# Kernel optimization log

Measured on AMD Instinct MI355X. Metric: run time of the kernel, lower is better.

The kernel has to match this reference:

```python
import jax, jax.numpy as jnp
import numpy as np

B, C, LO, LQ, H = 64, 4, 64, 128, 768
NEG = -10000.0


def _trilinear(u, um, v, vm, w1, b1, w2, b2, w3):
    # u: [N, Lu, H], v: [N, Lv, H]; returns [N, Lu, Lv]
    p1 = u @ w1 + b1                                  # [N, Lu, 1]
    p2 = (v @ w2 + b2).transpose(0, 2, 1)             # [N, 1, Lv]
    p3 = jnp.einsum('bud,bvd->buv', u * w3, v)        # trilinear term
    return p1 + p2 + p3 + ((1.0 - um) * NEG)[:, :, None] + ((1.0 - vm) * NEG)[:, None, :]


def _forward(encoded_o, encoded_q, om, qm,
             att_W1_w, att_W1_b, att_W2_w, att_W2_b, att_W3,
             Wc_self_w, Wc_self_b, Wc_w, Wc_b, Va_w, Va_b, Wg_w, Wg_b,
             co_W1_w, co_W1_b, co_W2_w, co_W2_b, co_W3, Wp_w, Wp_b,
             sa_W1_w, sa_W1_b, sa_W2_w, sa_W2_b, sa_W3, Wf_w, Wf_b):
    b, c, lo, h = encoded_o.shape
    lq = encoded_q.shape[2]
    p = c * (c - 1)
    # ---- pairwise option-compare (OCN_Att_layer) over all (i, j), j != i ----
    i_idx = np.repeat(np.arange(c), c - 1)
    j_idx = np.array([j for i in range(c) for j in range(c) if j != i])
    o_i = encoded_o[:, i_idx].reshape(b * p, lo, h)   # 'ok'
    o_j = encoded_o[:, j_idx].reshape(b * p, lo, h)   # 'ol'
    m_i = om[:, i_idx].reshape(b * p, lo)
    m_j = om[:, j_idx].reshape(b * p, lo)
    A = _trilinear(o_j, m_j, o_i, m_i, att_W1_w, att_W1_b, att_W2_w, att_W2_b, att_W3)
    att = jax.nn.softmax(A, axis=1)
    olk_ctx = jnp.einsum('bud,buv->bvd', o_j, att)    # [BP, LO, H]
    OLK = jnp.concatenate([o_i - olk_ctx, o_i * olk_ctx], axis=-1)  # [BP, LO, 2H]
    cmp_proj = OLK @ Wc_w + Wc_b                      # Wc applied per compare pair
    cmp_sum = cmp_proj.reshape(b, c, c - 1, lo, h).sum(axis=2).reshape(b * c, lo, h)
    # ---- merge layer (per candidate, flattened into batch) ----
    o1 = encoded_o.reshape(b * c, lo, h)
    q = encoded_q.reshape(b * c, lq, h)
    omf = om.reshape(b * c, lo)
    qmf = qm.reshape(b * c, lq)
    Aq = jax.nn.softmax(q @ Va_w + Va_b + ((1.0 - qmf) * NEG)[:, :, None], axis=1)  # [BC, LQ, 1]
    Q = jnp.einsum('bld,blo->bod', q, Aq)             # [BC, 1, H]
    OCK = jnp.tanh(o1 @ Wc_self_w + Wc_self_b + cmp_sum)
    Qb = jnp.broadcast_to(Q, (b * c, lo, h))
    G = jax.nn.sigmoid(jnp.concatenate([o1, OCK, Qb], axis=-1) @ Wg_w + Wg_b)
    merged = G * o1 + (1.0 - G) * OCK                 # [BC, LO, H]
    # ---- co-attention with question ----
    A2 = _trilinear(q, qmf, merged, omf, co_W1_w, co_W1_b, co_W2_w, co_W2_b, co_W3)  # [BC, LQ, LO]
    ACK = jax.nn.softmax(A2, axis=2)
    OA = jnp.einsum('bqo,bod->bqd', ACK, merged)      # [BC, LQ, H]
    APK = jax.nn.softmax(A2, axis=1)
    dOA = jnp.concatenate([q, OA], axis=-1)           # [BC, LQ, 2H]
    POAA = jnp.einsum('bqd,bqo->bod', dOA, APK)       # [BC, LO, 2H]
    OPK = jax.nn.relu(jnp.concatenate([merged, POAA], axis=-1) @ Wp_w + Wp_b)
    # ---- self-attention ----
    A3 = _trilinear(OPK, omf, OPK, omf, sa_W1_w, sa_W1_b, sa_W2_w, sa_W2_b, sa_W3)
    att3 = jax.nn.softmax(A3, axis=1)
    OSK = jnp.einsum('bud,buv->bvd', OPK, att3)
    OFK = jax.nn.relu(jnp.concatenate([OPK, OSK, OPK - OSK, OPK * OSK], axis=-1) @ Wf_w + Wf_b)
    return OFK.reshape(b, c, lo, h).max(axis=2)       # [B, C, H]


def setup_inputs():
    ks = jax.random.split(jax.random.key(0), 32)
    def p(i, shape, s=0.02):
        return jax.random.normal(ks[i], shape, jnp.float32) * s
    return {
        'encoded_o': jax.random.normal(ks[0], (B, C, LO, H), jnp.float32),
        'encoded_q': jax.random.normal(ks[1], (B, C, LQ, H), jnp.float32),
        'option_mask': jnp.ones((B, C, LO), jnp.int32),
        'question_mask': jnp.ones((B, C, LQ), jnp.int32),
        'att_W1_w': p(2, (H, 1)), 'att_W1_b': p(3, (1,)),
        'att_W2_w': p(4, (H, 1)), 'att_W2_b': p(5, (1,)),
        'att_W3': p(6, (H,)),
        'Wc_self_w': p(7, (H, H)), 'Wc_self_b': p(8, (H,)),
        'Wc_w': p(9, (2 * H, H)), 'Wc_b': p(10, (H,)),
        'Va_w': p(11, (H, 1)), 'Va_b': p(12, (1,)),
        'Wg_w': p(13, (3 * H, H)), 'Wg_b': p(14, (H,)),
        'co_W1_w': p(15, (H, 1)), 'co_W1_b': p(16, (1,)),
        'co_W2_w': p(17, (H, 1)), 'co_W2_b': p(18, (1,)),
        'co_W3': p(19, (H,)),
        'Wp_w': p(20, (3 * H, H)), 'Wp_b': p(21, (H,)),
        'sa_W1_w': p(22, (H, 1)), 'sa_W1_b': p(23, (1,)),
        'sa_W2_w': p(24, (H, 1)), 'sa_W2_b': p(25, (1,)),
        'sa_W3': p(26, (H,)),
        'Wf_w': p(27, (4 * H, H)), 'Wf_b': p(28, (H,)),
    }


def reference(encoded_o, encoded_q, option_mask, question_mask,
              att_W1_w, att_W1_b, att_W2_w, att_W2_b, att_W3,
              Wc_self_w, Wc_self_b, Wc_w, Wc_b, Va_w, Va_b, Wg_w, Wg_b,
              co_W1_w, co_W1_b, co_W2_w, co_W2_b, co_W3, Wp_w, Wp_b,
              sa_W1_w, sa_W1_b, sa_W2_w, sa_W2_b, sa_W3, Wf_w, Wf_b):
    return _forward(encoded_o, encoded_q,
                    option_mask.astype(jnp.float32), question_mask.astype(jnp.float32),
                    att_W1_w, att_W1_b, att_W2_w, att_W2_b, att_W3,
                    Wc_self_w, Wc_self_b, Wc_w, Wc_b, Va_w, Va_b, Wg_w, Wg_b,
                    co_W1_w, co_W1_b, co_W2_w, co_W2_b, co_W3, Wp_w, Wp_b,
                    sa_W1_w, sa_W1_b, sa_W2_w, sa_W2_b, sa_W3, Wf_w, Wf_b)
```

## Files before the change

### kernel.cpp

```cpp
#include <hip/hip_runtime.h>
#include <math.h>


#define NEGC (-10000.0f)
constexpr int HD = 768;

constexpr int EP_TANH = 1;
constexpr int EP_MERGE = 2;
constexpr int EP_RELU = 3;
constexpr int EP_RELU_MAX = 4;

typedef __attribute__((ext_vector_type(8))) short bf16x8;
typedef __attribute__((ext_vector_type(8))) unsigned short u16x8;
typedef __attribute__((ext_vector_type(4))) unsigned short u16x4;
typedef __attribute__((ext_vector_type(4))) float f32x4;

__device__ inline void st8(float* dst, float4 a0, float4 a1) {
  dst[0] = a0.x; dst[1] = a0.y; dst[2] = a0.z; dst[3] = a0.w;
  dst[4] = a1.x; dst[5] = a1.y; dst[6] = a1.z; dst[7] = a1.w;
}

__device__ inline unsigned short f2bf(float x) {
  unsigned int u = __float_as_uint(x);
  u += 0x7fffu + ((u >> 16) & 1u);
  return (unsigned short)(u >> 16);
}

__device__ inline float bf2f(unsigned short u) {
  return __uint_as_float(((unsigned int)u) << 16);
}

__device__ inline u16x8 pack8(float4 a, float4 b) {
  u16x8 r;
  r[0] = f2bf(a.x); r[1] = f2bf(a.y); r[2] = f2bf(a.z); r[3] = f2bf(a.w);
  r[4] = f2bf(b.x); r[5] = f2bf(b.y); r[6] = f2bf(b.z); r[7] = f2bf(b.w);
  return r;
}

__device__ inline void cvt8f(u16x8 v, float4& a, float4& b) {
  a.x = bf2f(v[0]); a.y = bf2f(v[1]); a.z = bf2f(v[2]); a.w = bf2f(v[3]);
  b.x = bf2f(v[4]); b.y = bf2f(v[5]); b.z = bf2f(v[6]); b.w = bf2f(v[7]);
}

__device__ inline void gload_lds16(const unsigned short* src, unsigned short* dst) {
  __builtin_amdgcn_global_load_lds(
      (const __attribute__((address_space(1))) void*)src,
      (__attribute__((address_space(3))) void*)dst, 16, 0, 0);
}

__global__ __launch_bounds__(256)
void dot768x2_bf16(const unsigned short* __restrict__ x,
                   const float* __restrict__ w1, const float* __restrict__ b1,
                   const float* __restrict__ w2, const float* __restrict__ b2,
                   float* __restrict__ o1, float* __restrict__ o2, int ntok) {
  int tok = blockIdx.x * 4 + (threadIdx.x >> 6);
  int lane = threadIdx.x & 63;
  if (tok >= ntok) return;
  const unsigned short* xp = x + (size_t)tok * HD;
  float s1 = 0.f, s2 = 0.f;
#pragma unroll
  for (int i = 0; i < 3; ++i) {
    int c = (lane + (i << 6)) << 2;
    u16x4 xv = *(const u16x4*)(xp + c);
    float4 wa = *(const float4*)(w1 + c);
    float4 wb = *(const float4*)(w2 + c);
    float x0 = bf2f(xv[0]), x1 = bf2f(xv[1]), x2 = bf2f(xv[2]), x3 = bf2f(xv[3]);
    s1 = fmaf(x0, wa.x, s1); s1 = fmaf(x1, wa.y, s1);
    s1 = fmaf(x2, wa.z, s1); s1 = fmaf(x3, wa.w, s1);
    s2 = fmaf(x0, wb.x, s2); s2 = fmaf(x1, wb.y, s2);
    s2 = fmaf(x2, wb.z, s2); s2 = fmaf(x3, wb.w, s2);
  }
#pragma unroll
  for (int off = 32; off; off >>= 1) {
    s1 += __shfl_xor(s1, off);
    s2 += __shfl_xor(s2, off);
  }
  if (lane == 0) { o1[tok] = s1 + b1[0]; o2[tok] = s2 + b2[0]; }
}

__global__ __launch_bounds__(256)
void dot768x2_f32(const float* __restrict__ x,
                  const float* __restrict__ w1, const float* __restrict__ b1,
                  const float* __restrict__ w2, const float* __restrict__ b2,
                  float* __restrict__ o1, float* __restrict__ o2, int ntok) {
  int tok = blockIdx.x * 4 + (threadIdx.x >> 6);
  int lane = threadIdx.x & 63;
  if (tok >= ntok) return;
  const float* xp = x + (size_t)tok * HD;
  float s1 = 0.f, s2 = 0.f;
#pragma unroll
  for (int i = 0; i < 3; ++i) {
    int c = (lane + (i << 6)) << 2;
    float4 xv = *(const float4*)(xp + c);
    float4 wa = *(const float4*)(w1 + c);
    float4 wb = *(const float4*)(w2 + c);
    s1 = fmaf(xv.x, wa.x, s1); s1 = fmaf(xv.y, wa.y, s1);
    s1 = fmaf(xv.z, wa.z, s1); s1 = fmaf(xv.w, wa.w, s1);
    s2 = fmaf(xv.x, wb.x, s2); s2 = fmaf(xv.y, wb.y, s2);
    s2 = fmaf(xv.z, wb.z, s2); s2 = fmaf(xv.w, wb.w, s2);
  }
#pragma unroll
  for (int off = 32; off; off >>= 1) {
    s1 += __shfl_xor(s1, off);
    s2 += __shfl_xor(s2, off);
  }
  if (lane == 0) { o1[tok] = s1 + b1[0]; o2[tok] = s2 + b2[0]; }
}

__global__ __launch_bounds__(256)
void dot768_bf16(const unsigned short* __restrict__ x,
                 const float* __restrict__ w1, const float* __restrict__ b1,
                 float* __restrict__ o1, int ntok) {
  int tok = blockIdx.x * 4 + (threadIdx.x >> 6);
  int lane = threadIdx.x & 63;
  if (tok >= ntok) return;
  const unsigned short* xp = x + (size_t)tok * HD;
  float s1 = 0.f;
#pragma unroll
  for (int i = 0; i < 3; ++i) {
    int c = (lane + (i << 6)) << 2;
    u16x4 xv = *(const u16x4*)(xp + c);
    float4 wa = *(const float4*)(w1 + c);
    s1 = fmaf(bf2f(xv[0]), wa.x, s1); s1 = fmaf(bf2f(xv[1]), wa.y, s1);
    s1 = fmaf(bf2f(xv[2]), wa.z, s1); s1 = fmaf(bf2f(xv[3]), wa.w, s1);
  }
#pragma unroll
  for (int off = 32; off; off >>= 1) s1 += __shfl_xor(s1, off);
  if (lane == 0) o1[tok] = s1 + b1[0];
}

__global__ void bias_ock_kernel(const float* __restrict__ b1, const float* __restrict__ b2,
                                float* __restrict__ o) {
  int n = blockIdx.x * 256 + threadIdx.x;
  if (n < HD) o[n] = b1[n] + 3.f * b2[n];
}

__global__ __launch_bounds__(256)
void bfprep_kernel(const float* __restrict__ x, const float* __restrict__ w3,
                   unsigned short* __restrict__ xbf, unsigned short* __restrict__ xw3) {
  size_t base = ((size_t)blockIdx.x * 256 + threadIdx.x) * 8;
  int col = (int)(base % HD);
  float4 a0 = *(const float4*)(x + base);
  float4 a1 = *(const float4*)(x + base + 4);
  float4 w0 = *(const float4*)(w3 + col);
  float4 w1 = *(const float4*)(w3 + col + 4);
  *(u16x8*)(xbf + base) = pack8(a0, a1);
  float4 s0, s1;
  s0.x = a0.x * w0.x; s0.y = a0.y * w0.y; s0.z = a0.z * w0.z; s0.w = a0.w * w0.w;
  s1.x = a1.x * w1.x; s1.y = a1.y * w1.y; s1.z = a1.z * w1.z; s1.w = a1.w * w1.w;
  *(u16x8*)(xw3 + base) = pack8(s0, s1);
}

__global__ __launch_bounds__(256)
void w3scale_bf16(const unsigned short* __restrict__ x, const float* __restrict__ w3,
                  unsigned short* __restrict__ xw3) {
  size_t base = ((size_t)blockIdx.x * 256 + threadIdx.x) * 8;
  int col = (int)(base % HD);
  u16x8 v = *(const u16x8*)(x + base);
  float4 a, b;
  cvt8f(v, a, b);
  float4 w0 = *(const float4*)(w3 + col);
  float4 w1 = *(const float4*)(w3 + col + 4);
  a.x *= w0.x; a.y *= w0.y; a.z *= w0.z; a.w *= w0.w;
  b.x *= w1.x; b.y *= w1.y; b.z *= w1.z; b.w *= w1.w;
  *(u16x8*)(xw3 + base) = pack8(a, b);
}

template<int M1>
__global__ __launch_bounds__(256)
void modeprep_kernel(const unsigned short* __restrict__ a, const unsigned short* __restrict__ b,
                     unsigned short* __restrict__ y1, unsigned short* __restrict__ y2) {
  size_t base = ((size_t)blockIdx.x * 256 + threadIdx.x) * 8;
  u16x8 av = *(const u16x8*)(a + base);
  u16x8 bv = *(const u16x8*)(b + base);
  float4 a0, a1, b0, b1;
  cvt8f(av, a0, a1);
  cvt8f(bv, b0, b1);
  float4 p0, p1, q0, q1;
  if (M1 == 1) {
    p0.x = fmaf(3.f, a0.x, -b0.x); p0.y = fmaf(3.f, a0.y, -b0.y);
    p0.z = fmaf(3.f, a0.z, -b0.z); p0.w = fmaf(3.f, a0.w, -b0.w);
    p1.x = fmaf(3.f, a1.x, -b1.x); p1.y = fmaf(3.f, a1.y, -b1.y);
    p1.z = fmaf(3.f, a1.z, -b1.z); p1.w = fmaf(3.f, a1.w, -b1.w);
  } else {
    p0.x = a0.x - b0.x; p0.y = a0.y - b0.y; p0.z = a0.z - b0.z; p0.w = a0.w - b0.w;
    p1.x = a1.x - b1.x; p1.y = a1.y - b1.y; p1.z = a1.z - b1.z; p1.w = a1.w - b1.w;
  }
  q0.x = a0.x * b0.x; q0.y = a0.y * b0.y; q0.z = a0.z * b0.z; q0.w = a0.w * b0.w;
  q1.x = a1.x * b1.x; q1.y = a1.y * b1.y; q1.z = a1.z * b1.z; q1.w = a1.w * b1.w;
  *(u16x8*)(y1 + base) = pack8(p0, p1);
  *(u16x8*)(y2 + base) = pack8(q0, q1);
}

template<int NJ>
__global__ __launch_bounds__(256)
void p1_kernel(const unsigned short* __restrict__ Xbf, const unsigned short* __restrict__ Xw3,
               const float* __restrict__ s1g, const float* __restrict__ s2g,
               const int* __restrict__ maskg, unsigned short* __restrict__ PtG) {
  __shared__ __align__(16) unsigned short Ua[64 * 136];
  __shared__ __align__(16) unsigned short Vb[64 * 136];
  __shared__ float Sbuf[64][66];
  __shared__ float red[4][64];
  const int t = threadIdx.x;
  int ubc, vbc;
  if (NJ == 1) {
    ubc = vbc = blockIdx.x;
  } else {
    const int b = blockIdx.x / 12, pr = blockIdx.x % 12;
    const int i = pr / 3, jj = pr % 3;
    const int j = jj + (jj >= i ? 1 : 0);
    vbc = (b << 2) + i; ubc = (b << 2) + j;
  }
  const unsigned short* U = Xbf + (size_t)ubc * (64 * HD);
  const unsigned short* V = Xw3 + (size_t)vbc * (64 * HD);
  const int w = t >> 6, lane = t & 63, l15 = lane & 15, l4 = lane >> 4;
  const int srow = t >> 2, scol = (t & 3) << 5;
  f32x4 acc[4] = {};
  for (int k0 = 0; k0 < HD; k0 += 128) {
    const unsigned short* up = U + (size_t)srow * HD + k0 + scol;
    const unsigned short* vp = V + (size_t)srow * HD + k0 + scol;
    unsigned short* ua = &Ua[srow * 136 + scol];
    unsigned short* vb = &Vb[srow * 136 + scol];
#pragma unroll
    for (int z = 0; z < 4; ++z) {
      *(u16x8*)(ua + z * 8) = *(const u16x8*)(up + z * 8);
      *(u16x8*)(vb + z * 8) = *(const u16x8*)(vp + z * 8);
    }
    __syncthreads();
#pragma unroll
    for (int ks = 0; ks < 4; ++ks) {
      bf16x8 af = *(const bf16x8*)(&Ua[(w * 16 + l15) * 136 + ks * 32 + l4 * 8]);
#pragma unroll
      for (int n = 0; n < 4; ++n) {
        bf16x8 bf = *(const bf16x8*)(&Vb[(n * 16 + l15) * 136 + ks * 32 + l4 * 8]);
        acc[n] = __builtin_amdgcn_mfma_f32_16x16x32_bf16(af, bf, acc[n], 0, 0, 0);
      }
    }
    __syncthreads();
  }
  {
    float s1v[4];
#pragma unroll
    for (int r = 0; r < 4; ++r) {
      int u = w * 16 + l4 * 4 + r;
      s1v[r] = s1g[ubc * 64 + u] + (1.f - (float)maskg[ubc * 64 + u]) * NEGC;
    }
#pragma unroll
    for (int n = 0; n < 4; ++n) {
      int v = n * 16 + l15;
      float s2v = s2g[vbc * 64 + v] + (1.f - (float)maskg[vbc * 64 + v]) * NEGC;
#pragma unroll
      for (int r = 0; r < 4; ++r)
        Sbuf[w * 16 + l4 * 4 + r][v] = acc[n][r] + s1v[r] + s2v;
    }
  }
  __syncthreads();
  {
    const int v = t & 63, part = t >> 6;
    float m = -1e30f;
#pragma unroll
    for (int z = 0; z < 16; ++z) m = fmaxf(m, Sbuf[part * 16 + z][v]);
    red[part][v] = m;
    __syncthreads();
    float gm = fmaxf(fmaxf(red[0][v], red[1][v]), fmaxf(red[2][v], red[3][v]));
    float s = 0.f;
#pragma unroll
    for (int z = 0; z < 16; ++z) {
      float e = expf(Sbuf[part * 16 + z][v] - gm);
      Sbuf[part * 16 + z][v] = e;
      s += e;
    }
    __syncthreads();
    red[part][v] = s;
    __syncthreads();
    float cinv = 1.f / (red[0][v] + red[1][v] + red[2][v] + red[3][v]);
    unsigned short* pt = PtG + (size_t)blockIdx.x * 4096 + v * 64 + part * 16;
#pragma unroll
    for (int z = 0; z < 16; ++z) pt[z] = f2bf(Sbuf[part * 16 + z][v] * cinv);
  }
}

template<int NJ>
__global__ __launch_bounds__(256)
void p2_kernel(const unsigned short* __restrict__ Xbf, const unsigned short* __restrict__ PtG,
               unsigned short* __restrict__ outg) {
  __shared__ __align__(16) unsigned short Pts[NJ][64 * 72];
  __shared__ __align__(16) unsigned short U2[64 * 192];
  const int t = threadIdx.x;
  const int dq = blockIdx.x, bc = blockIdx.y;
  const int d0 = dq * 192;
  const int b = bc >> 2, i = bc & 3;
  const int w = t >> 6, lane = t & 63, l15 = lane & 15, l4 = lane >> 4;
  {
    const int v = t >> 2, cs = (t & 3) << 4;
#pragma unroll
    for (int jj = 0; jj < NJ; ++jj) {
      size_t src = (NJ == 1 ? (size_t)bc : (size_t)(b * 12 + i * 3 + jj)) * 4096 + v * 64 + cs;
      *(u16x8*)(&Pts[jj][v * 72 + cs]) = *(const u16x8*)(PtG + src);
      *(u16x8*)(&Pts[jj][v * 72 + cs + 8]) = *(const u16x8*)(PtG + src + 8);
    }
  }
  f32x4 acc[4][3] = {};
  const int su = t >> 2, sc0 = (t & 3) * 48;
  const int sswz = ((su >> 3) & 3) << 5;
  for (int jj = 0; jj < NJ; ++jj) {
    const int ubc = (NJ == 1) ? bc : ((b << 2) + (jj + (jj >= i ? 1 : 0)));
    __syncthreads();
    {
      const unsigned short* up = Xbf + (size_t)ubc * (64 * HD) + (size_t)su * HD + d0 + sc0;
#pragma unroll
      for (int it = 0; it < 6; ++it) {
        u16x8 vdat = *(const u16x8*)(up + it * 8);
        *(u16x8*)((char*)U2 + ((su * 384 + (sc0 + it * 8) * 2) ^ sswz)) = vdat;
      }
    }
    __syncthreads();
    const unsigned short* ptj = &Pts[jj][0];
#pragma unroll
    for (int ks = 0; ks < 2; ++ks) {
      bf16x8 bfr[3];
#pragma unroll
      for (int n = 0; n < 3; ++n) {
        const int col = (w * 3 + n) * 16 + l15;
#pragma unroll
        for (int e = 0; e < 8; ++e) {
          const int uk = ks * 32 + l4 * 8 + e;
          const int byte = (uk * 384 + col * 2) ^ (((uk >> 3) & 3) << 5);
          bfr[n][e] = *(const short*)((const char*)U2 + byte);
        }
      }
#pragma unroll
      for (int m = 0; m < 4; ++m) {
        bf16x8 af = *(const bf16x8*)(ptj + (m * 16 + l15) * 72 + ks * 32 + l4 * 8);
#pragma unroll
        for (int n = 0; n < 3; ++n)
          acc[m][n] = __builtin_amdgcn_mfma_f32_16x16x32_bf16(af, bfr[n], acc[m][n], 0, 0, 0);
      }
    }
  }
  unsigned short* op = outg + (size_t)bc * (64 * HD);
#pragma unroll
  for (int m = 0; m < 4; ++m)
#pragma unroll
    for (int n = 0; n < 3; ++n) {
      const int d = d0 + (w * 3 + n) * 16 + l15;
#pragma unroll
      for (int r = 0; r < 4; ++r) {
        const int v = m * 16 + l4 * 4 + r;
        op[(size_t)v * HD + d] = f2bf(acc[m][n][r]);
      }
    }
}

__global__ __launch_bounds__(256)
void qpool_kernel(const float* __restrict__ q, const float* __restrict__ qa,
                  const int* __restrict__ qm, float* __restrict__ Q) {
  __shared__ float wgt[128];
  __shared__ float wred[4];
  int t = threadIdx.x, bc = blockIdx.x;
  const float* qap = qa + bc * 128;
  const int* qmp = qm + bc * 128;
  float v = -1e30f;
  if (t < 128) v = qap[t] + (1.f - (float)qmp[t]) * NEGC;
  float m = v;
#pragma unroll
  for (int off = 32; off; off >>= 1) m = fmaxf(m, __shfl_xor(m, off));
  if ((t & 63) == 0) wred[t >> 6] = m;
  __syncthreads();
  float gm = fmaxf(fmaxf(wred[0], wred[1]), fmaxf(wred[2], wred[3]));
  float e = (t < 128) ? expf(v - gm) : 0.f;
  float s = e;
#pragma unroll
  for (int off = 32; off; off >>= 1) s += __shfl_xor(s, off);
  __syncthreads();
  if ((t & 63) == 0) wred[t >> 6] = s;
  __syncthreads();
  float tot = wred[0] + wred[1] + wred[2] + wred[3];
  if (t < 128) wgt[t] = e / tot;
  __syncthreads();
  const float* qp = q + (size_t)bc * (128 * HD);
  float* Qp = Q + (size_t)bc * HD;
  for (int d = t; d < HD; d += 256) {
    float acc = 0.f;
    for (int l = 0; l < 128; ++l) acc = fmaf(wgt[l], qp[(size_t)l * HD + d], acc);
    Qp[d] = acc;
  }
}

__global__ __launch_bounds__(256)
void a2_mfma_kernel(const float* __restrict__ qin, const unsigned short* __restrict__ mergedb,
                    const float* __restrict__ qco1, const float* __restrict__ ms2,
                    const int* __restrict__ qm, const int* __restrict__ om,
                    const float* __restrict__ w3, float* __restrict__ A2) {
  __shared__ __align__(16) unsigned short Aq[128 * 72];
  __shared__ __align__(16) unsigned short Bm[64 * 72];
  const int t = threadIdx.x, bc = blockIdx.x;
  const float* qp = qin + (size_t)bc * (128 * HD);
  const unsigned short* mp = mergedb + (size_t)bc * (64 * HD);
  const int w = t >> 6, lane = t & 63, l15 = lane & 15, l4 = lane >> 4;
  const int arow = t >> 1, acs = (t & 1) << 5;
  const int brow = t >> 2, bcs = (t & 3) << 4;
  f32x4 acc[2][4] = {};
  for (int k0 = 0; k0 < HD; k0 += 64) {
    {
      const float* p = qp + (size_t)arow * HD + k0 + acs;
      const float* wp = w3 + k0 + acs;
      unsigned short* dst = &Aq[arow * 72 + acs];
#pragma unroll
      for (int z = 0; z < 4; ++z) {
        float4 a = *(const float4*)(p + z * 8);
        float4 b = *(const float4*)(p + z * 8 + 4);
        float4 wa = *(const float4*)(wp + z * 8);
        float4 wb = *(const float4*)(wp + z * 8 + 4);
        a.x *= wa.x; a.y *= wa.y; a.z *= wa.z; a.w *= wa.w;
        b.x *= wb.x; b.y *= wb.y; b.z *= wb.z; b.w *= wb.w;
        *(u16x8*)(dst + z * 8) = pack8(a, b);
      }
    }
    {
      const unsigned short* p = mp + (size_t)brow * HD + k0 + bcs;
      unsigned short* dst = &Bm[brow * 72 + bcs];
      *(u16x8*)(dst) = *(const u16x8*)(p);
      *(u16x8*)(dst + 8) = *(const u16x8*)(p + 8);
    }
    __syncthreads();
#pragma unroll
    for (int ks = 0; ks < 2; ++ks) {
      bf16x8 af[2], bf[4];
#pragma unroll
      for (int m = 0; m < 2; ++m)
        af[m] = *(const bf16x8*)(&Aq[(w * 32 + m * 16 + l15) * 72 + ks * 32 + l4 * 8]);
#pragma unroll
      for (int n = 0; n < 4; ++n)
        bf[n] = *(const bf16x8*)(&Bm[(n * 16 + l15) * 72 + ks * 32 + l4 * 8]);
#pragma unroll
      for (int m = 0; m < 2; ++m)
#pragma unroll
        for (int n = 0; n < 4; ++n)
          acc[m][n] = __builtin_amdgcn_mfma_f32_16x16x32_bf16(af[m], bf[n], acc[m][n], 0, 0, 0);
    }
    __syncthreads();
  }
  const float* qc = qco1 + bc * 128;
  const int* qmp = qm + bc * 128;
  const float* msp = ms2 + bc * 64;
  const int* omp = om + bc * 64;
  float* outp = A2 + (size_t)bc * (128 * 64);
#pragma unroll
  for (int n = 0; n < 4; ++n) {
    const int v = n * 16 + l15;
    const float ct = msp[v] + (1.f - (float)omp[v]) * NEGC;
#pragma unroll
    for (int m = 0; m < 2; ++m)
#pragma unroll
      for (int r = 0; r < 4; ++r) {
        const int qrow = w * 32 + m * 16 + l4 * 4 + r;
        const float rt = qc[qrow] + (1.f - (float)qmp[qrow]) * NEGC;
        outp[qrow * 64 + v] = acc[m][n][r] + rt + ct;
      }
  }
}

__global__ __launch_bounds__(256)
void poaa_mfma_kernel(const float* __restrict__ A2, const float* __restrict__ qin,
                      const unsigned short* __restrict__ mergedb,
                      unsigned short* __restrict__ PLO, unsigned short* __restrict__ PHI) {
  __shared__ __align__(16) char smem[77312];
  __shared__ float red[4][64];
  __shared__ float rowm[128], rowfac[128];
  __shared__ float colfac[64];
  __shared__ float gmax_s;
  float* T = (float*)smem;
  unsigned short* Tt = (unsigned short*)(smem + 33280);
  unsigned short* Tft = (unsigned short*)(smem + 50688);
  unsigned short* M2bf = (unsigned short*)(smem + 68096);
  unsigned short* Qc = (unsigned short*)smem;
  unsigned short* Mc = (unsigned short*)(smem + 18432);

  const int t = threadIdx.x, bc = blockIdx.x;
  const int w = t >> 6, lane = t & 63, l15 = lane & 15, l4 = lane >> 4;
  const float* a2 = A2 + (size_t)bc * (128 * 64);
  {
    int row = t >> 1, cs = (t & 1) << 5;
    const float* p = a2 + row * 64 + cs;
#pragma unroll
    for (int z = 0; z < 8; ++z) {
      float4 v = *(const float4*)(p + (z << 2));
      T[row * 65 + cs + (z << 2) + 0] = v.x;
      T[row * 65 + cs + (z << 2) + 1] = v.y;
      T[row * 65 + cs + (z << 2) + 2] = v.z;
      T[row * 65 + cs + (z << 2) + 3] = v.w;
    }
  }
  __syncthreads();
  {
    int qrow = t >> 1, h = t & 1;
    float m = -1e30f;
    for (int v = h * 32; v < h * 32 + 32; ++v) m = fmaxf(m, T[qrow * 65 + v]);
    m = fmaxf(m, __shfl_xor(m, 1));
    float s = 0.f;
    for (int v = h * 32; v < h * 32 + 32; ++v) s += expf(T[qrow * 65 + v] - m);
    s += __shfl_xor(s, 1);
    if (h == 0) { rowm[qrow] = m; rowfac[qrow] = s; }
  }
  float colm_loc = 0.f;
  {
    int v = t & 63, part = t >> 6;
    float m = -1e30f;
    for (int qq = part * 32; qq < part * 32 + 32; ++qq) m = fmaxf(m, T[qq * 65 + v]);
    red[part][v] = m;
    __syncthreads();
    float cm = fmaxf(fmaxf(red[0][v], red[1][v]), fmaxf(red[2][v], red[3][v]));
    float s = 0.f;
    for (int qq = part * 32; qq < part * 32 + 32; ++qq) s += expf(T[qq * 65 + v] - cm);
    __syncthreads();
    red[part][v] = s;
    __syncthreads();
    if (part == 0) { colm_loc = cm; colfac[v] = red[0][v] + red[1][v] + red[2][v] + red[3][v]; }
  }
  __syncthreads();
  if (t < 64) {
    float m = fmaxf(rowm[t], rowm[t + 64]);
#pragma unroll
    for (int off = 32; off; off >>= 1) m = fmaxf(m, __shfl_xor(m, off));
    if (t == 0) gmax_s = m;
  }
  __syncthreads();
  const float gmax = gmax_s;
  if (t < 128) rowfac[t] = expf(fminf(gmax - rowm[t], 60.f)) / rowfac[t];
  if (t < 64) colfac[t] = expf(fminf(gmax - colm_loc, 60.f)) / colfac[t];
  __syncthreads();
  {
    const int o = t >> 2, qs = (t & 3) << 5;
    for (int z = 0; z < 32; ++z) {
      const int qq = qs + z;
      float e = expf(T[qq * 65 + o] - gmax);
      Tt[o * 136 + qq] = f2bf(e);
      Tft[o * 136 + qq] = f2bf(e * rowfac[qq]);
    }
  }
  __syncthreads();
  {
    f32x4 m2acc[4] = {};
#pragma unroll
    for (int ks = 0; ks < 4; ++ks) {
      bf16x8 af = *(const bf16x8*)(&Tt[(w * 16 + l15) * 136 + ks * 32 + l4 * 8]);
#pragma unroll
      for (int n = 0; n < 4; ++n) {
        bf16x8 bf = *(const bf16x8*)(&Tft[(n * 16 + l15) * 136 + ks * 32 + l4 * 8]);
        m2acc[n] = __builtin_amdgcn_mfma_f32_16x16x32_bf16(af, bf, m2acc[n], 0, 0, 0);
      }
    }
#pragma unroll
    for (int n = 0; n < 4; ++n)
#pragma unroll
      for (int r = 0; r < 4; ++r) {
        const int o = w * 16 + l4 * 4 + r;
        M2bf[o * 72 + n * 16 + l15] = f2bf(colfac[o] * m2acc[n][r]);
      }
  }
  const int dql = t >> 1, dqs = (t & 1) << 5;
  const int dml = t >> 2, dms = (t & 3) << 4;
  const int swq = ((dql >> 3) & 3) << 5;
  const int swm = ((dml >> 3) & 3) << 5;
  unsigned short* plo = PLO + (size_t)bc * (64 * HD);
  unsigned short* phi = PHI + (size_t)bc * (64 * HD);
  const float* qp = qin + (size_t)bc * (128 * HD);
  const unsigned short* mp = mergedb + (size_t)bc * (64 * HD);
  for (int dc = 0; dc < 12; ++dc) {
    const int d0 = dc * 64;
    __syncthreads();
    {
      const float* p = qp + (size_t)dql * HD + d0 + dqs;
#pragma unroll
      for (int z = 0; z < 4; ++z) {
        float4 a = *(const float4*)(p + z * 8);
        float4 b = *(const float4*)(p + z * 8 + 4);
        *(u16x8*)((char*)Qc + ((dql * 144 + (dqs + z * 8) * 2) ^ swq)) = pack8(a, b);
      }
    }
    {
      const unsigned short* p = mp + (size_t)dml * HD + d0 + dms;
      *(u16x8*)((char*)Mc + ((dml * 144 + dms * 2) ^ swm)) = *(const u16x8*)p;
      *(u16x8*)((char*)Mc + ((dml * 144 + (dms + 8) * 2) ^ swm)) = *(const u16x8*)(p + 8);
    }
    __syncthreads();
    const int col = w * 16 + l15;
    f32x4 lacc[4] = {};
#pragma unroll
    for (int ks = 0; ks < 4; ++ks) {
      bf16x8 bf;
#pragma unroll
      for (int e = 0; e < 8; ++e) {
        const int qq = ks * 32 + l4 * 8 + e;
        bf[e] = *(const short*)((const char*)Qc + ((qq * 144 + col * 2) ^ (((qq >> 3) & 3) << 5)));
      }
#pragma unroll
      for (int m = 0; m < 4; ++m) {
        bf16x8 af = *(const bf16x8*)(&Tt[(m * 16 + l15) * 136 + ks * 32 + l4 * 8]);
        lacc[m] = __builtin_amdgcn_mfma_f32_16x16x32_bf16(af, bf, lacc[m], 0, 0, 0);
      }
    }
    f32x4 pacc[4] = {};
#pragma unroll
    for (int ks = 0; ks < 2; ++ks) {
      bf16x8 bf;
#pragma unroll
      for (int e = 0; e < 8; ++e) {
        const int vv = ks * 32 + l4 * 8 + e;
        bf[e] = *(const short*)((const char*)Mc + ((vv * 144 + col * 2) ^ (((vv >> 3) & 3) << 5)));
      }
#pragma unroll
      for (int m = 0; m < 4; ++m) {
        bf16x8 af = *(const bf16x8*)(&M2bf[(m * 16 + l15) * 72 + ks * 32 + l4 * 8]);
        pacc[m] = __builtin_amdgcn_mfma_f32_16x16x32_bf16(af, bf, pacc[m], 0, 0, 0);
      }
    }
#pragma unroll
    for (int m = 0; m < 4; ++m)
#pragma unroll
      for (int r = 0; r < 4; ++r) {
        const int o = m * 16 + l4 * 4 + r;
        const int d = d0 + w * 16 + l15;
        plo[(size_t)o * HD + d] = f2bf(colfac[o] * lacc[m][r]);
        phi[(size_t)o * HD + d] = f2bf(pacc[m][r]);
      }
  }
}

struct GemmArgs {
  const float* a[4];
  const float* w[4];
  int nchunks;
  const float* bias;
  float* out;
};

__global__ __launch_bounds__(256)
void gemm_store_kernel(GemmArgs g) {
  __shared__ float As[64][33];
  __shared__ float Ws[32][65];
  const int t = threadIdx.x;
  const int m0 = blockIdx.y << 6, n0 = blockIdx.x << 6;
  const int tr = t >> 4, tc = t & 15;
  float acc[4][4];
#pragma unroll
  for (int x = 0; x < 4; ++x)
#pragma unroll
    for (int y = 0; y < 4; ++y) acc[x][y] = 0.f;
  const int arow = t >> 2, acs = (t & 3) << 3;
  const int wrow = t >> 3, wcs = (t & 7) << 3;
  for (int c = 0; c < g.nchunks; ++c) {
// ... 167 lines not shown
      for (int r = 0; r < 4; ++r) {
        const int row = m0 + wr * 64 + mi * 16 + l4 * 4 + r;
#pragma unroll
        for (int ni = 0; ni < 4; ++ni) {
          const int n = n0 + wc * 64 + ni * 16 + l15;
          const size_t oi = (size_t)row * HD + n;
          float v = acc[mi][ni][r];
          if (EP == EP_TANH) {
            g.outb[oi] = f2bf(tanhf(v + g.bias[n]));
          } else if (EP == EP_MERGE) {
            float gg = v + g.aux2[(size_t)(row >> 6) * HD + n];
            float sg = 1.f / (1.f + expf(-gg));
            float o1v = bf2f(g.aux0[oi]);
            float ock = bf2f(g.aux1[oi]);
            g.outb[oi] = f2bf(fmaf(sg, o1v - ock, ock));
          } else {
            g.outb[oi] = f2bf(fmaxf(v + g.bias[n], 0.f));
          }
        }
      }
  }
}

extern "C" void kernel_launch(void* const* d_in, const int* in_sizes, int n_in,
                              void* d_out, int out_size, void* d_ws, size_t ws_size,
                              hipStream_t stream) {
  const float* enc_o = (const float*)d_in[0];
  const float* enc_q = (const float*)d_in[1];
  const int* om = (const int*)d_in[2];
  const int* qm = (const int*)d_in[3];
  const float* att_W1_w = (const float*)d_in[4];
  const float* att_W1_b = (const float*)d_in[5];
  const float* att_W2_w = (const float*)d_in[6];
  const float* att_W2_b = (const float*)d_in[7];
  const float* att_W3 = (const float*)d_in[8];
  const float* Wc_self_w = (const float*)d_in[9];
  const float* Wc_self_b = (const float*)d_in[10];
  const float* Wc_w = (const float*)d_in[11];
  const float* Wc_b = (const float*)d_in[12];
  const float* Va_w = (const float*)d_in[13];
  const float* Va_b = (const float*)d_in[14];
  const float* Wg_w = (const float*)d_in[15];
  const float* Wg_b = (const float*)d_in[16];
  const float* co_W1_w = (const float*)d_in[17];
  const float* co_W1_b = (const float*)d_in[18];
  const float* co_W2_w = (const float*)d_in[19];
  const float* co_W2_b = (const float*)d_in[20];
  const float* co_W3 = (const float*)d_in[21];
  const float* Wp_w = (const float*)d_in[22];
  const float* Wp_b = (const float*)d_in[23];
  const float* sa_W1_w = (const float*)d_in[24];
  const float* sa_W1_b = (const float*)d_in[25];
  const float* sa_W2_w = (const float*)d_in[26];
  const float* sa_W2_b = (const float*)d_in[27];
  const float* sa_W3 = (const float*)d_in[28];
  const float* Wf_w = (const float*)d_in[29];
  const float* Wf_b = (const float*)d_in[30];
  float* out = (float*)d_out;

  const int NTOK_O = 16384;
  const int NTOK_Q = 32768;
  const int HH = 768 * 768;

  float* ws = (float*)d_ws;
  size_t off = 0;
  auto carve = [&](size_t n) { float* p = ws + off; off += n; return p; };
  float* s1o   = carve(16384);
  float* s2o   = carve(16384);
  float* qa    = carve(32768);
  float* qco1  = carve(32768);
  float* ms2   = carve(16384);
  float* sa1   = carve(16384);
  float* sa2   = carve(16384);
  float* biasO = carve(1024);
  float* Qpool = carve(196608);
  float* Qg    = carve(196608);
  float* A2buf = carve(2097152);
  float* r1 = carve(12582912);
  float* r2 = carve(12582912);
  float* r3 = carve(12582912);
  float* r4 = carve(12582912);
  unsigned short* wtb = (unsigned short*)carve(1179648);
  if (ws_size < off * sizeof(float)) return;
  unsigned short* CSb   = (unsigned short*)r1;
  unsigned short* OPKb  = (unsigned short*)r1;
  unsigned short* X1    = (unsigned short*)(r1 + 6291456);
  unsigned short* X3    = (unsigned short*)(r1 + 6291456);
  unsigned short* OCKb  = (unsigned short*)r2;
  unsigned short* PLOb  = (unsigned short*)r2;
  unsigned short* opkw3 = (unsigned short*)r2;
  unsigned short* X2    = (unsigned short*)(r2 + 6291456);
  unsigned short* MRGb  = (unsigned short*)r3;
  unsigned short* OSKb  = (unsigned short*)r3;
  unsigned short* X4    = (unsigned short*)(r3 + 6291456);
  unsigned short* eobf  = (unsigned short*)r4;
  unsigned short* eow3  = (unsigned short*)(r4 + 6291456);
  unsigned short* PHIb  = (unsigned short*)r4;
  unsigned short* PtG   = (unsigned short*)A2buf;

  const dim3 GBIG(128, 6);
  const int PREP_GRID = NTOK_O * HD / (256 * 8);

  bfprep_kernel<<<PREP_GRID, 256, 0, stream>>>(enc_o, att_W3, eobf, eow3);
  dot768x2_bf16<<<NTOK_O / 4, 256, 0, stream>>>(eobf, att_W1_w, att_W1_b,
                                                att_W2_w, att_W2_b, s1o, s2o, NTOK_O);
  dot768x2_f32<<<NTOK_Q / 4, 256, 0, stream>>>(enc_q, Va_w, Va_b,
                                               co_W1_w, co_W1_b, qa, qco1, NTOK_Q);
  bias_ock_kernel<<<3, 256, 0, stream>>>(Wc_self_b, Wc_b, biasO);

  p1_kernel<3><<<768, 256, 0, stream>>>(eobf, eow3, s1o, s2o, om, PtG);
  p2_kernel<3><<<dim3(4, 256), 256, 0, stream>>>(eobf, PtG, CSb);

  {
    modeprep_kernel<1><<<PREP_GRID, 256, 0, stream>>>(eobf, CSb, X1, X2);
    WcArgs wa{};
    wa.src[0] = Wc_self_w; wa.src[1] = Wc_w; wa.src[2] = Wc_w + HH;
    wa.dst = wtb; wa.Kw = 2304;
    wconv_kernel<<<dim3(144, 3), 256, 0, stream>>>(wa);
    MMArgs g{};
    g.a[0] = eobf; g.a[1] = X1; g.a[2] = X2;
    g.K = 2304; g.wt = wtb; g.bias = biasO; g.outb = OCKb;
    mfma_gemm_kernel<EP_TANH><<<GBIG, 256, 0, stream>>>(g);
  }

  qpool_kernel<<<256, 256, 0, stream>>>(enc_q, qa, qm, Qpool);
  {
    GemmArgs g{};
    g.a[0] = Qpool; g.w[0] = Wg_w + 2 * HH;
    g.nchunks = 1; g.bias = Wg_b; g.out = Qg;
    gemm_store_kernel<<<dim3(12, 4), 256, 0, stream>>>(g);
  }

  {
    WcArgs wa{};
    wa.src[0] = Wg_w; wa.src[1] = Wg_w + HH;
    wa.dst = wtb; wa.Kw = 1536;
    wconv_kernel<<<dim3(144, 2), 256, 0, stream>>>(wa);
    MMArgs g{};
    g.a[0] = eobf; g.a[1] = OCKb;
    g.K = 1536; g.wt = wtb; g.bias = nullptr;
    g.aux0 = eobf; g.aux1 = OCKb; g.aux2 = Qg; g.outb = MRGb;
    mfma_gemm_kernel<EP_MERGE><<<GBIG, 256, 0, stream>>>(g);
  }

  dot768_bf16<<<NTOK_O / 4, 256, 0, stream>>>(MRGb, co_W2_w, co_W2_b, ms2, NTOK_O);
  a2_mfma_kernel<<<256, 256, 0, stream>>>(enc_q, MRGb, qco1, ms2, qm, om, co_W3, A2buf);
  poaa_mfma_kernel<<<256, 256, 0, stream>>>(A2buf, enc_q, MRGb, PLOb, PHIb);

  {
    WcArgs wa{};
    wa.src[0] = Wp_w; wa.src[1] = Wp_w + HH; wa.src[2] = Wp_w + 2 * HH;
    wa.dst = wtb; wa.Kw = 2304;
    wconv_kernel<<<dim3(144, 3), 256, 0, stream>>>(wa);
    MMArgs g{};
    g.a[0] = MRGb; g.a[1] = PLOb; g.a[2] = PHIb;
    g.K = 2304; g.wt = wtb; g.bias = Wp_b; g.outb = OPKb;
    mfma_gemm_kernel<EP_RELU><<<GBIG, 256, 0, stream>>>(g);
  }

  dot768x2_bf16<<<NTOK_O / 4, 256, 0, stream>>>(OPKb, sa_W1_w, sa_W1_b,
                                                sa_W2_w, sa_W2_b, sa1, sa2, NTOK_O);
  w3scale_bf16<<<PREP_GRID, 256, 0, stream>>>(OPKb, sa_W3, opkw3);
  p1_kernel<1><<<256, 256, 0, stream>>>(OPKb, opkw3, sa1, sa2, om, PtG);
  p2_kernel<1><<<dim3(4, 256), 256, 0, stream>>>(OPKb, PtG, OSKb);

  {
    modeprep_kernel<3><<<PREP_GRID, 256, 0, stream>>>(OPKb, OSKb, X3, X4);
    WcArgs wa{};
    wa.src[0] = Wf_w; wa.src[1] = Wf_w + HH; wa.src[2] = Wf_w + 2 * HH; wa.src[3] = Wf_w + 3 * HH;
    wa.dst = wtb; wa.Kw = 3072;
    wconv_kernel<<<dim3(144, 4), 256, 0, stream>>>(wa);
    MMArgs g{};
    g.a[0] = OPKb; g.a[1] = OSKb; g.a[2] = X3; g.a[3] = X4;
    g.K = 3072; g.wt = wtb; g.bias = Wf_b; g.outf = out;
    mfma_gemm_kernel<EP_RELU_MAX><<<GBIG, 256, 0, stream>>>(g);
  }
}
```

Baseline: 659.7 us.

## Fuse prep, dot and mode-prep kernels into neighbours; split a2/poaa grids

The bf16 conversion and W3 scaling are merged with the dot-product kernel, and the W3 scaling of OPK is merged with its dot kernel. The modeprep elementwise pass is folded into the p2 epilogue, so p2 writes the difference and product tensors directly instead of an intermediate that is re-read. The a2 and poaa kernels are split over two blocks per batch item to double the grid. This cuts kernel launches and global round-trips, but p2 now does scattered scalar stores and reads Oi per element.

```diff
diff --git a/kernel.cpp b/kernel.cpp
--- a/kernel.cpp
+++ b/kernel.cpp
@@ -37,9 +37,10 @@
   return r;
 }
 
-__device__ inline void cvt8f(u16x8 v, float4& a, float4& b) {
-  a.x = bf2f(v[0]); a.y = bf2f(v[1]); a.z = bf2f(v[2]); a.w = bf2f(v[3]);
-  b.x = bf2f(v[4]); b.y = bf2f(v[5]); b.z = bf2f(v[6]); b.w = bf2f(v[7]);
+__device__ inline u16x4 pack4(float4 a) {
+  u16x4 r;
+  r[0] = f2bf(a.x); r[1] = f2bf(a.y); r[2] = f2bf(a.z); r[3] = f2bf(a.w);
+  return r;
 }
 
 __device__ inline void gload_lds16(const unsigned short* src, unsigned short* dst) {
@@ -49,26 +50,70 @@
 }
 
 __global__ __launch_bounds__(256)
-void dot768x2_bf16(const unsigned short* __restrict__ x,
-                   const float* __restrict__ w1, const float* __restrict__ b1,
-                   const float* __restrict__ w2, const float* __restrict__ b2,
-                   float* __restrict__ o1, float* __restrict__ o2, int ntok) {
+void bfprep_dot_kernel(const float* __restrict__ x, const float* __restrict__ w3,
+                       const float* __restrict__ w1, const float* __restrict__ b1,
+                       const float* __restrict__ w2, const float* __restrict__ b2,
+                       unsigned short* __restrict__ xbf, unsigned short* __restrict__ xw3,
+                       float* __restrict__ o1, float* __restrict__ o2, int ntok) {
+  int tok = blockIdx.x * 4 + (threadIdx.x >> 6);
+  int lane = threadIdx.x & 63;
+  if (tok >= ntok) return;
+  const float* xp = x + (size_t)tok * HD;
+  unsigned short* xb = xbf + (size_t)tok * HD;
+  unsigned short* xw = xw3 + (size_t)tok * HD;
+  float s1 = 0.f, s2 = 0.f;
+#pragma unroll
+  for (int i = 0; i < 3; ++i) {
+    int c = (lane + (i << 6)) << 2;
+    float4 xv = *(const float4*)(xp + c);
+    float4 w3v = *(const float4*)(w3 + c);
+    float4 wa = *(const float4*)(w1 + c);
+    float4 wb = *(const float4*)(w2 + c);
+    s1 = fmaf(xv.x, wa.x, s1); s1 = fmaf(xv.y, wa.y, s1);
+    s1 = fmaf(xv.z, wa.z, s1); s1 = fmaf(xv.w, wa.w, s1);
+    s2 = fmaf(xv.x, wb.x, s2); s2 = fmaf(xv.y, wb.y, s2);
+    s2 = fmaf(xv.z, wb.z, s2); s2 = fmaf(xv.w, wb.w, s2);
+    *(u16x4*)(xb + c) = pack4(xv);
+    float4 sv;
+    sv.x = xv.x * w3v.x; sv.y = xv.y * w3v.y; sv.z = xv.z * w3v.z; sv.w = xv.w * w3v.w;
+    *(u16x4*)(xw + c) = pack4(sv);
+  }
+#pragma unroll
+  for (int off = 32; off; off >>= 1) {
+    s1 += __shfl_xor(s1, off);
+    s2 += __shfl_xor(s2, off);
+  }
+  if (lane == 0) { o1[tok] = s1 + b1[0]; o2[tok] = s2 + b2[0]; }
+}
+
+__global__ __launch_bounds__(256)
+void opkprep_kernel(const unsigned short* __restrict__ x, const float* __restrict__ w3,
+                    const float* __restrict__ w1, const float* __restrict__ b1,
+                    const float* __restrict__ w2, const float* __restrict__ b2,
+                    unsigned short* __restrict__ xw3,
+                    float* __restrict__ o1, float* __restrict__ o2, int ntok) {
   int tok = blockIdx.x * 4 + (threadIdx.x >> 6);
   int lane = threadIdx.x & 63;
   if (tok >= ntok) return;
   const unsigned short* xp = x + (size_t)tok * HD;
+  unsigned short* xw = xw3 + (size_t)tok * HD;
   float s1 = 0.f, s2 = 0.f;
 #pragma unroll
   for (int i = 0; i < 3; ++i) {
     int c = (lane + (i << 6)) << 2;
     u16x4 xv = *(const u16x4*)(xp + c);
+    float x0 = bf2f(xv[0]), x1 = bf2f(xv[1]), x2 = bf2f(xv[2]), x3 = bf2f(xv[3]);
+    float4 w3v = *(const float4*)(w3 + c);
     float4 wa = *(const float4*)(w1 + c);
     float4 wb = *(const float4*)(w2 + c);
-    float x0 = bf2f(xv[0]), x1 = bf2f(xv[1]), x2 = bf2f(xv[2]), x3 = bf2f(xv[3]);
     s1 = fmaf(x0, wa.x, s1); s1 = fmaf(x1, wa.y, s1);
     s1 = fmaf(x2, wa.z, s1); s1 = fmaf(x3, wa.w, s1);
     s2 = fmaf(x0, wb.x, s2); s2 = fmaf(x1, wb.y, s2);
     s2 = fmaf(x2, wb.z, s2); s2 = fmaf(x3, wb.w, s2);
+    u16x4 sv;
+    sv[0] = f2bf(x0 * w3v.x); sv[1] = f2bf(x1 * w3v.y);
+    sv[2] = f2bf(x2 * w3v.z); sv[3] = f2bf(x3 * w3v.w);
+    *(u16x4*)(xw + c) = sv;
   }
 #pragma unroll
   for (int off = 32; off; off >>= 1) {
@@ -133,63 +178,6 @@
                                 float* __restrict__ o) {
   int n = blockIdx.x * 256 + threadIdx.x;
   if (n < HD) o[n] = b1[n] + 3.f * b2[n];
-}
-
-__global__ __launch_bounds__(256)
-void bfprep_kernel(const float* __restrict__ x, const float* __restrict__ w3,
-                   unsigned short* __restrict__ xbf, unsigned short* __restrict__ xw3) {
-  size_t base = ((size_t)blockIdx.x * 256 + threadIdx.x) * 8;
-  int col = (int)(base % HD);
-  float4 a0 = *(const float4*)(x + base);
-  float4 a1 = *(const float4*)(x + base + 4);
-  float4 w0 = *(const float4*)(w3 + col);
-  float4 w1 = *(const float4*)(w3 + col + 4);
-  *(u16x8*)(xbf + base) = pack8(a0, a1);
-  float4 s0, s1;
-  s0.x = a0.x * w0.x; s0.y = a0.y * w0.y; s0.z = a0.z * w0.z; s0.w = a0.w * w0.w;
-  s1.x = a1.x * w1.x; s1.y = a1.y * w1.y; s1.z = a1.z * w1.z; s1.w = a1.w * w1.w;
-  *(u16x8*)(xw3 + base) = pack8(s0, s1);
-}
-
-__global__ __launch_bounds__(256)
-void w3scale_bf16(const unsigned short* __restrict__ x, const float* __restrict__ w3,
-                  unsigned short* __restrict__ xw3) {
-  size_t base = ((size_t)blockIdx.x * 256 + threadIdx.x) * 8;
-  int col = (int)(base % HD);
-  u16x8 v = *(const u16x8*)(x + base);
-  float4 a, b;
-  cvt8f(v, a, b);
-  float4 w0 = *(const float4*)(w3 + col);
-  float4 w1 = *(const float4*)(w3 + col + 4);
-  a.x *= w0.x; a.y *= w0.y; a.z *= w0.z; a.w *= w0.w;
-  b.x *= w1.x; b.y *= w1.y; b.z *= w1.z; b.w *= w1.w;
-  *(u16x8*)(xw3 + base) = pack8(a, b);
-}
-
-template<int M1>
-__global__ __launch_bounds__(256)
-void modeprep_kernel(const unsigned short* __restrict__ a, const unsigned short* __restrict__ b,
-                     unsigned short* __restrict__ y1, unsigned short* __restrict__ y2) {
-  size_t base = ((size_t)blockIdx.x * 256 + threadIdx.x) * 8;
-  u16x8 av = *(const u16x8*)(a + base);
-  u16x8 bv = *(const u16x8*)(b + base);
-  float4 a0, a1, b0, b1;
-  cvt8f(av, a0, a1);
-  cvt8f(bv, b0, b1);
-  float4 p0, p1, q0, q1;
-  if (M1 == 1) {
-    p0.x = fmaf(3.f, a0.x, -b0.x); p0.y = fmaf(3.f, a0.y, -b0.y);
-    p0.z = fmaf(3.f, a0.z, -b0.z); p0.w = fmaf(3.f, a0.w, -b0.w);
-    p1.x = fmaf(3.f, a1.x, -b1.x); p1.y = fmaf(3.f, a1.y, -b1.y);
-    p1.z = fmaf(3.f, a1.z, -b1.z); p1.w = fmaf(3.f, a1.w, -b1.w);
-  } else {
-    p0.x = a0.x - b0.x; p0.y = a0.y - b0.y; p0.z = a0.z - b0.z; p0.w = a0.w - b0.w;
-    p1.x = a1.x - b1.x; p1.y = a1.y - b1.y; p1.z = a1.z - b1.z; p1.w = a1.w - b1.w;
-  }
-  q0.x = a0.x * b0.x; q0.y = a0.y * b0.y; q0.z = a0.z * b0.z; q0.w = a0.w * b0.w;
-  q1.x = a1.x * b1.x; q1.y = a1.y * b1.y; q1.z = a1.z * b1.z; q1.w = a1.w * b1.w;
-  *(u16x8*)(y1 + base) = pack8(p0, p1);
-  *(u16x8*)(y2 + base) = pack8(q0, q1);
 }
 
 template<int NJ>
@@ -283,7 +271,9 @@
 template<int NJ>
 __global__ __launch_bounds__(256)
 void p2_kernel(const unsigned short* __restrict__ Xbf, const unsigned short* __restrict__ PtG,
-               unsigned short* __restrict__ outg) {
+               const unsigned short* __restrict__ Oi,
+               unsigned short* __restrict__ osk,
+               unsigned short* __restrict__ y1, unsigned short* __restrict__ y2) {
   __shared__ __align__(16) unsigned short Pts[NJ][64 * 72];
   __shared__ __align__(16) unsigned short U2[64 * 192];
   const int t = threadIdx.x;
@@ -338,7 +328,8 @@
       }
     }
   }
-  unsigned short* op = outg + (size_t)bc * (64 * HD);
+  const unsigned short* oip = Oi + (size_t)bc * (64 * HD);
+  const size_t obase = (size_t)bc * (64 * HD);
 #pragma unroll
   for (int m = 0; m < 4; ++m)
 #pragma unroll
@@ -347,7 +338,17 @@
 #pragma unroll
       for (int r = 0; r < 4; ++r) {
         const int v = m * 16 + l4 * 4 + r;
-        op[(size_t)v * HD + d] = f2bf(acc[m][n][r]);
+        const size_t idx = obase + (size_t)v * HD + d;
+        const float cs = acc[m][n][r];
+        const float oi = bf2f(oip[(size_t)v * HD + d]);
+        if (NJ == 3) {
+          y1[idx] = f2bf(fmaf(3.f, oi, -cs));
+          y2[idx] = f2bf(oi * cs);
+        } else {
+          osk[idx] = f2bf(cs);
+          y1[idx] = f2bf(oi - cs);
+          y2[idx] = f2bf(oi * cs);
+        }
       }
     }
 }
@@ -392,22 +393,21 @@
                     const float* __restrict__ qco1, const float* __restrict__ ms2,
                     const int* __restrict__ qm, const int* __restrict__ om,
                     const float* __restrict__ w3, float* __restrict__ A2) {
-  __shared__ __align__(16) unsigned short Aq[128 * 72];
+  __shared__ __align__(16) unsigned short Aq[64 * 72];
   __shared__ __align__(16) unsigned short Bm[64 * 72];
-  const int t = threadIdx.x, bc = blockIdx.x;
-  const float* qp = qin + (size_t)bc * (128 * HD);
+  const int t = threadIdx.x, qh = blockIdx.x, bc = blockIdx.y;
+  const float* qp = qin + (size_t)bc * (128 * HD) + (size_t)(qh * 64) * HD;
   const unsigned short* mp = mergedb + (size_t)bc * (64 * HD);
   const int w = t >> 6, lane = t & 63, l15 = lane & 15, l4 = lane >> 4;
-  const int arow = t >> 1, acs = (t & 1) << 5;
-  const int brow = t >> 2, bcs = (t & 3) << 4;
-  f32x4 acc[2][4] = {};
+  const int srow = t >> 2, scs = (t & 3) << 4;
+  f32x4 acc[4] = {};
   for (int k0 = 0; k0 < HD; k0 += 64) {
     {
-      const float* p = qp + (size_t)arow * HD + k0 + acs;
-      const float* wp = w3 + k0 + acs;
-      unsigned short* dst = &Aq[arow * 72 + acs];
-#pragma unroll
-      for (int z = 0; z < 4; ++z) {
+      const float* p = qp + (size_t)srow * HD + k0 + scs;
+      const float* wp = w3 + k0 + scs;
+      unsigned short* dst = &Aq[srow * 72 + scs];
+#pragma unroll
+      for (int z = 0; z < 2; ++z) {
         float4 a = *(const float4*)(p + z * 8);
         float4 b = *(const float4*)(p + z * 8 + 4);
         float4 wa = *(const float4*)(wp + z * 8);
@@ -418,26 +418,20 @@
       }
     }
     {
-      const unsigned short* p = mp + (size_t)brow * HD + k0 + bcs;
-      unsigned short* dst = &Bm[brow * 72 + bcs];
+      const unsigned short* p = mp + (size_t)srow * HD + k0 + scs;
+      unsigned short* dst = &Bm[srow * 72 + scs];
       *(u16x8*)(dst) = *(const u16x8*)(p);
       *(u16x8*)(dst + 8) = *(const u16x8*)(p + 8);
     }
     __syncthreads();
 #pragma unroll
     for (int ks = 0; ks < 2; ++ks) {
-      bf16x8 af[2], bf[4];
-#pragma unroll
-      for (int m = 0; m < 2; ++m)
-        af[m] = *(const bf16x8*)(&Aq[(w * 32 + m * 16 + l15) * 72 + ks * 32 + l4 * 8]);
-#pragma unroll
-      for (int n = 0; n < 4; ++n)
-        bf[n] = *(const bf16x8*)(&Bm[(n * 16 + l15) * 72 + ks * 32 + l4 * 8]);
-#pragma unroll
-      for (int m = 0; m < 2; ++m)
-#pragma unroll
-        for (int n = 0; n < 4; ++n)
-          acc[m][n] = __builtin_amdgcn_mfma_f32_16x16x32_bf16(af[m], bf[n], acc[m][n], 0, 0, 0);
+      bf16x8 af = *(const bf16x8*)(&Aq[(w * 16 + l15) * 72 + ks * 32 + l4 * 8]);
+#pragma unroll
+      for (int n = 0; n < 4; ++n) {
+        bf16x8 bf = *(const bf16x8*)(&Bm[(n * 16 + l15) * 72 + ks * 32 + l4 * 8]);
+        acc[n] = __builtin_amdgcn_mfma_f32_16x16x32_bf16(af, bf, acc[n], 0, 0, 0);
+      }
     }
     __syncthreads();
   }
@@ -445,19 +439,18 @@
   const int* qmp = qm + bc * 128;
   const float* msp = ms2 + bc * 64;
   const int* omp = om + bc * 64;
-  float* outp = A2 + (size_t)bc * (128 * 64);
+  float* outp = A2 + (size_t)bc * (128 * 64) + (size_t)(qh * 64) * 64;
 #pragma unroll
   for (int n = 0; n < 4; ++n) {
     const int v = n * 16 + l15;
     const float ct = msp[v] + (1.f - (float)omp[v]) * NEGC;
 #pragma unroll
-    for (int m = 0; m < 2; ++m)
-#pragma unroll
-      for (int r = 0; r < 4; ++r) {
-        const int qrow = w * 32 + m * 16 + l4 * 4 + r;
-        const float rt = qc[qrow] + (1.f - (float)qmp[qrow]) * NEGC;
-        outp[qrow * 64 + v] = acc[m][n][r] + rt + ct;
-      }
+    for (int r = 0; r < 4; ++r) {
+      const int ql = w * 16 + l4 * 4 + r;
+      const int qrow = qh * 64 + ql;
+      const float rt = qc[qrow] + (1.f - (float)qmp[qrow]) * NEGC;
+      outp[ql * 64 + v] = acc[n][r] + rt + ct;
+    }
   }
 }
 
@@ -477,7 +470,7 @@
   unsigned short* Qc = (unsigned short*)smem;
   unsigned short* Mc = (unsigned short*)(smem + 18432);
 
-  const int t = threadIdx.x, bc = blockIdx.x;
+  const int t = threadIdx.x, dqh = blockIdx.x, bc = blockIdx.y;
   const int w = t >> 6, lane = t & 63, l15 = lane & 15, l4 = lane >> 4;
   const float* a2 = A2 + (size_t)bc * (128 * 64);
   {
@@ -567,7 +560,7 @@
   unsigned short* phi = PHI + (size_t)bc * (64 * HD);
   const float* qp = qin + (size_t)bc * (128 * HD);
   const unsigned short* mp = mergedb + (size_t)bc * (64 * HD);
-  for (int dc = 0; dc < 12; ++dc) {
+  for (int dc = dqh * 6; dc < dqh * 6 + 6; ++dc) {
     const int d0 = dc * 64;
     __syncthreads();
     {
@@ -901,7 +894,6 @@
   float* r4 = carve(12582912);
   unsigned short* wtb = (unsigned short*)carve(1179648);
   if (ws_size < off * sizeof(float)) return;
-  unsigned short* CSb   = (unsigned short*)r1;
   unsigned short* OPKb  = (unsigned short*)r1;
   unsigned short* X1    = (unsigned short*)(r1 + 6291456);
   unsigned short* X3    = (unsigned short*)(r1 + 6291456);
@@ -918,20 +910,18 @@
   unsigned short* PtG   = (unsigned short*)A2buf;
 
   const dim3 GBIG(128, 6);
-  const int PREP_GRID = NTOK_O * HD / (256 * 8);
-
-  bfprep_kernel<<<PREP_GRID, 256, 0, stream>>>(enc_o, att_W3, eobf, eow3);
-  dot768x2_bf16<<<NTOK_O / 4, 256, 0, stream>>>(eobf, att_W1_w, att_W1_b,
-                                                att_W2_w, att_W2_b, s1o, s2o, NTOK_O);
+
+  bfprep_dot_kernel<<<NTOK_O / 4, 256, 0, stream>>>(enc_o, att_W3, att_W1_w, att_W1_b,
+                                                    att_W2_w, att_W2_b, eobf, eow3,
+                                                    s1o, s2o, NTOK_O);
   dot768x2_f32<<<NTOK_Q / 4, 256, 0, stream>>>(enc_q, Va_w, Va_b,
                                                co_W1_w, co_W1_b, qa, qco1, NTOK_Q);
   bias_ock_kernel<<<3, 256, 0, stream>>>(Wc_self_b, Wc_b, biasO);
 
   p1_kernel<3><<<768, 256, 0, stream>>>(eobf, eow3, s1o, s2o, om, PtG);
-  p2_kernel<3><<<dim3(4, 256), 256, 0, stream>>>(eobf, PtG, CSb);
-
-  {
-    modeprep_kernel<1><<<PREP_GRID, 256, 0, stream>>>(eobf, CSb, X1, X2);
+  p2_kernel<3><<<dim3(4, 256), 256, 0, stream>>>(eobf, PtG, eobf, nullptr, X1, X2);
+
+  {
     WcArgs wa{};
     wa.src[0] = Wc_self_w; wa.src[1] = Wc_w; wa.src[2] = Wc_w + HH;
     wa.dst = wtb; wa.Kw = 2304;
@@ -963,8 +953,8 @@
   }
 
   dot768_bf16<<<NTOK_O / 4, 256, 0, stream>>>(MRGb, co_W2_w, co_W2_b, ms2, NTOK_O);
-  a2_mfma_kernel<<<256, 256, 0, stream>>>(enc_q, MRGb, qco1, ms2, qm, om, co_W3, A2buf);
-  poaa_mfma_kernel<<<256, 256, 0, stream>>>(A2buf, enc_q, MRGb, PLOb, PHIb);
+  a2_mfma_kernel<<<dim3(2, 256), 256, 0, stream>>>(enc_q, MRGb, qco1, ms2, qm, om, co_W3, A2buf);
+  poaa_mfma_kernel<<<dim3(2, 256), 256, 0, stream>>>(A2buf, enc_q, MRGb, PLOb, PHIb);
 
   {
     WcArgs wa{};
@@ -977,14 +967,12 @@
     mfma_gemm_kernel<EP_RELU><<<GBIG, 256, 0, stream>>>(g);
   }
 
-  dot768x2_bf16<<<NTOK_O / 4, 256, 0, stream>>>(OPKb, sa_W1_w, sa_W1_b,
-                                                sa_W2_w, sa_W2_b, sa1, sa2, NTOK_O);
-  w3scale_bf16<<<PREP_GRID, 256, 0, stream>>>(OPKb, sa_W3, opkw3);
+  opkprep_kernel<<<NTOK_O / 4, 256, 0, stream>>>(OPKb, sa_W3, sa_W1_w, sa_W1_b,
+                                                 sa_W2_w, sa_W2_b, opkw3, sa1, sa2, NTOK_O);
   p1_kernel<1><<<256, 256, 0, stream>>>(OPKb, opkw3, sa1, sa2, om, PtG);
-  p2_kernel<1><<<dim3(4, 256), 256, 0, stream>>>(OPKb, PtG, OSKb);
-
-  {
-    modeprep_kernel<3><<<PREP_GRID, 256, 0, stream>>>(OPKb, OSKb, X3, X4);
+  p2_kernel<1><<<dim3(4, 256), 256, 0, stream>>>(OPKb, PtG, OPKb, OSKb, X3, X4);
+
+  {
     WcArgs wa{};
     wa.src[0] = Wf_w; wa.src[1] = Wf_w + HH; wa.src[2] = Wf_w + 2 * HH; wa.src[3] = Wf_w + 3 * HH;
     wa.dst = wtb; wa.Kw = 3072;
```

Result: faster. 619.7 us (-6.1%).
